# Optimization experiments

Measured on AMD Instinct MI355X. Metric: run time of the kernel, lower is better.

## Reference

```python
import jax, jax.numpy as jnp
import numpy as np

EMBED = 384
HEADS = 6
HEAD_SIZE = EMBED // HEADS
EPS = 1e-5


def _layernorm(x, g, b):
    mu = jnp.mean(x, axis=-1, keepdims=True)
    var = jnp.mean(jnp.square(x - mu), axis=-1, keepdims=True)
    return (x - mu) * jax.lax.rsqrt(var + EPS) * g + b


def setup_inputs() -> dict:
    key = jax.random.key(0)
    ks = jax.random.split(key, 16)
    B, T = 64, 256
    s_in = 1.0 / np.sqrt(EMBED)
    return {
        "x": jax.random.normal(ks[0], (B, T, EMBED), dtype=jnp.float32),
        # per-head q/k/v projections, stacked over heads: [H, C, D]
        "Wq": jax.random.normal(ks[1], (HEADS, EMBED, HEAD_SIZE), dtype=jnp.float32) * s_in,
        "bq": jnp.zeros((HEADS, HEAD_SIZE), dtype=jnp.float32),
        "Wk": jax.random.normal(ks[2], (HEADS, EMBED, HEAD_SIZE), dtype=jnp.float32) * s_in,
        "bk": jnp.zeros((HEADS, HEAD_SIZE), dtype=jnp.float32),
        "Wv": jax.random.normal(ks[3], (HEADS, EMBED, HEAD_SIZE), dtype=jnp.float32) * s_in,
        "bv": jnp.zeros((HEADS, HEAD_SIZE), dtype=jnp.float32),
        "Wp": jax.random.normal(ks[4], (EMBED, EMBED), dtype=jnp.float32) * s_in,
        "bp": jnp.zeros((EMBED,), dtype=jnp.float32),
        "W1": jax.random.normal(ks[5], (EMBED, EMBED), dtype=jnp.float32) * s_in,
        "b1": jnp.zeros((EMBED,), dtype=jnp.float32),
        "W2": jax.random.normal(ks[6], (EMBED, EMBED), dtype=jnp.float32) * s_in,
        "b2": jnp.zeros((EMBED,), dtype=jnp.float32),
        "ln1_g": jnp.ones((EMBED,), dtype=jnp.float32),
        "ln1_b": jnp.zeros((EMBED,), dtype=jnp.float32),
        "ln2_g": jnp.ones((EMBED,), dtype=jnp.float32),
        "ln2_b": jnp.zeros((EMBED,), dtype=jnp.float32),
    }


def reference(x, Wq, bq, Wk, bk, Wv, bv, Wp, bp, W1, b1, W2, b2,
              ln1_g, ln1_b, ln2_g, ln2_b):
    B, T, C = x.shape
    h = _layernorm(x, ln1_g, ln1_b)
    # batched per-head projections: [B,H,T,D]
    q = jnp.einsum('btc,hcd->bhtd', h, Wq) + bq[None, :, None, :]
    k = jnp.einsum('btc,hcd->bhtd', h, Wk) + bk[None, :, None, :]
    v = jnp.einsum('btc,hcd->bhtd', h, Wv) + bv[None, :, None, :]
    # NOTE: original scales by embed_size**0.5 (C=384), not head_size.
    wei = jnp.einsum('bhtd,bhsd->bhts', q, k) / jnp.sqrt(jnp.float32(C))
    causal = jnp.tril(jnp.ones((T, T), dtype=bool))
    wei = jnp.where(causal[None, None], wei, -jnp.inf)
    wei = jax.nn.softmax(wei, axis=-1)  # dropout = identity in eval
    attn = jnp.einsum('bhts,bhsd->bhtd', wei, v)  # [B,H,T,D]
    # concat heads in head order -> [B,T,C]
    attn = attn.transpose(0, 2, 1, 3).reshape(B, T, C)
    x = x + attn @ Wp + bp
    h2 = _layernorm(x, ln2_g, ln2_b)
    ff = jax.nn.relu(h2 @ W1 + b1) @ W2 + b2
    return x + ff
```

## Files before the change

### kernel.cpp

```cpp
#include <hip/hip_runtime.h>

typedef _Float16 f16;
typedef _Float16 half8 __attribute__((ext_vector_type(8)));
typedef _Float16 half4v __attribute__((ext_vector_type(4)));
typedef float floatx4 __attribute__((ext_vector_type(4)));

#define B_ 64
#define T_ 256
#define C_ 384
#define H_ 6
#define D_ 64
#define NROWS (B_*T_)

typedef __attribute__((address_space(3))) void lds_void_t;
typedef const __attribute__((address_space(1))) void gvoid_t;

__device__ __forceinline__ void g2lds16(const void* g, void* l) {
  __builtin_amdgcn_global_load_lds((gvoid_t*)g, (lds_void_t*)l, 16, 0, 0);
}

__global__ __launch_bounds__(256) void prep_ln_kernel(
    const float* __restrict__ Wq, const float* __restrict__ Wk, const float* __restrict__ Wv,
    const float* __restrict__ bq, const float* __restrict__ bk, const float* __restrict__ bv,
    const float* __restrict__ Wp, const float* __restrict__ W1, const float* __restrict__ W2,
    f16* __restrict__ Wqkv_t, f16* __restrict__ Wp_t, f16* __restrict__ W1_t, f16* __restrict__ W2_t,
    float* __restrict__ bqkv,
    const float* __restrict__ x, const float* __restrict__ gamma, const float* __restrict__ beta,
    f16* __restrict__ hout)
{
  const int bid = blockIdx.x;
  const int tid = threadIdx.x;
  if (bid >= 217) {
    int row = (bid - 217) * 4 + (tid >> 6);
    int lane = tid & 63;
    const float* xr = x + (size_t)row * 384;
    float v[6]; float s = 0.f;
#pragma unroll
    for (int j = 0; j < 6; j++) { v[j] = xr[lane + 64*j]; s += v[j]; }
#pragma unroll
    for (int m = 1; m < 64; m <<= 1) s += __shfl_xor(s, m);
    float mu = s * (1.f/384.f);
    float var = 0.f;
#pragma unroll
    for (int j = 0; j < 6; j++) { float d = v[j]-mu; var += d*d; }
#pragma unroll
    for (int m = 1; m < 64; m <<= 1) var += __shfl_xor(var, m);
    float rs = rsqrtf(var * (1.f/384.f) + 1e-5f);
    f16* orow = hout + (size_t)row*384;
#pragma unroll
    for (int j = 0; j < 6; j++) {
      int col = lane + 64*j;
      orow[col] = (f16)((v[j]-mu)*rs*gamma[col] + beta[col]);
    }
    return;
  }
  if (bid == 216) {
    for (int i = tid; i < 1152; i += 256) {
      float v;
      if (i < 384)      v = bq[i];
      else if (i < 768) v = bk[i - 384];
      else              v = bv[i - 768];
      bqkv[i] = v;
    }
    return;
  }
  __shared__ __align__(16) float tile[64*68];
  const float* src; int srcStride; f16* dst;
  if (bid < 108) {
    int mat = bid / 36, rem = bid - mat*36;
    int h = rem / 6, kt = rem - h*6;
    const float* W = (mat == 0) ? Wq : (mat == 1) ? Wk : Wv;
    src = W + (size_t)(h*384 + kt*64)*64;
    srcStride = 64;
    dst = Wqkv_t + (size_t)(mat*384 + h*64)*384 + kt*64;
  } else {
    int b2 = bid - 108;
    int mat = b2 / 36, rem = b2 - mat*36;
    int kt = rem / 6, ct = rem - kt*6;
    const float* W = (mat == 0) ? Wp : (mat == 1) ? W1 : W2;
    src = W + (size_t)(kt*64)*384 + ct*64;
    srcStride = 384;
    f16* O = (mat == 0) ? Wp_t : (mat == 1) ? W1_t : W2_t;
    dst = O + (size_t)(ct*64)*384 + kt*64;
  }
#pragma unroll
  for (int i = 0; i < 4; i++) {
    int idx = i*256 + tid;
    int r = idx >> 4, c4 = idx & 15;
    float4 v = *(const float4*)(src + (size_t)r*srcStride + c4*4);
    *(float4*)(&tile[r*68 + c4*4]) = v;
  }
  __syncthreads();
#pragma unroll
  for (int i = 0; i < 4; i++) {
    int idx = i*256 + tid;
    int d = idx >> 4, k4 = idx & 15;
    half4v o;
#pragma unroll
    for (int j = 0; j < 4; j++) o[j] = (f16)tile[(k4*4 + j)*68 + d];
    *(half4v*)(dst + (size_t)d*384 + k4*4) = o;
  }
}

__global__ __launch_bounds__(256) void gemm_qkv_kernel(
    const f16* __restrict__ A, const f16* __restrict__ Bt,
    const float* __restrict__ bias, f16* __restrict__ outp, int ldo)
{
  __shared__ __align__(16) f16 As[2][128*32];
  __shared__ __align__(16) f16 Bs[2][128*32];
  const int tid = threadIdx.x;
  const int lane = tid & 63, w = tid >> 6;
  const int wm = w >> 1, wn = w & 1;
  const int q = lane >> 4, c15 = lane & 15;
  const long row0 = (long)blockIdx.x * 128;
  const long col0 = (long)blockIdx.y * 128;
  floatx4 acc[4][4] = {};

  const int c0 = tid,        r0c = c0 >> 2, p0 = c0 & 3, g0 = p0 ^ ((r0c >> 1) & 3);
  const int c1 = 256 + tid,  r1c = c1 >> 2, p1 = c1 & 3, g1 = p1 ^ ((r1c >> 1) & 3);
  const f16* Arow0 = A  + (row0 + r0c)*384 + g0*8;
  const f16* Arow1 = A  + (row0 + r1c)*384 + g1*8;
  const f16* Brow0 = Bt + (col0 + r0c)*384 + g0*8;
  const f16* Brow1 = Bt + (col0 + r1c)*384 + g1*8;
  const int dof0 = (w*64)*8, dof1 = (256 + w*64)*8;

  for (int k0 = 0; k0 < 384; k0 += 64) {
#pragma unroll
    for (int hf = 0; hf < 2; hf++) {
      int kk = k0 + hf*32;
      g2lds16(Arow0 + kk, &As[hf][dof0]);
      g2lds16(Arow1 + kk, &As[hf][dof1]);
      g2lds16(Brow0 + kk, &Bs[hf][dof0]);
      g2lds16(Brow1 + kk, &Bs[hf][dof1]);
    }
    __syncthreads();
#pragma unroll
    for (int hf = 0; hf < 2; hf++) {
      half8 af[4], bf[4];
#pragma unroll
      for (int mi = 0; mi < 4; mi++) {
        int r = wm*64 + mi*16 + c15;
        int ph = q ^ ((r >> 1) & 3);
        af[mi] = *(const half8*)(&As[hf][r*32 + ph*8]);
      }
#pragma unroll
      for (int ni = 0; ni < 4; ni++) {
        int r = wn*64 + ni*16 + c15;
        int ph = q ^ ((r >> 1) & 3);
        bf[ni] = *(const half8*)(&Bs[hf][r*32 + ph*8]);
      }
#pragma unroll
      for (int mi = 0; mi < 4; mi++)
#pragma unroll
        for (int ni = 0; ni < 4; ni++)
          acc[mi][ni] = __builtin_amdgcn_mfma_f32_16x16x32_f16(af[mi], bf[ni], acc[mi][ni], 0, 0, 0);
    }
    __syncthreads();
  }

#pragma unroll
  for (int ni = 0; ni < 4; ni++) {
    long col = col0 + wn*64 + ni*16 + c15;
    float bv = bias[col];
#pragma unroll
    for (int mi = 0; mi < 4; mi++) {
      long rowb = row0 + wm*64 + mi*16 + q*4;
#pragma unroll
      for (int r = 0; r < 4; r++) {
        float vo = acc[mi][ni][r] + bv;
        outp[(rowb + r) * (long)ldo + col] = (f16)vo;
      }
    }
  }
}

__global__ __launch_bounds__(512, 2) void attn_kernel(const f16* __restrict__ qkv,
                                                      f16* __restrict__ attn_out)
{
  __shared__ __align__(16) char kvbuf[32768];
  __shared__ __align__(16) f16 Pbuf[8][16*64];
  f16* Ks = (f16*)kvbuf;
  unsigned int* vTw = (unsigned int*)kvbuf;
  f16* vT = (f16*)kvbuf;

  const int tid = threadIdx.x;
  const int bid = blockIdx.x;
  const int bh = bid >> 1, qt2 = bid & 1;
  const int b = bh / 6, h = bh - b*6;
  const f16* qp = qkv + (size_t)b*256*1152 + h*64;
  const f16* kp = qp + 384;
  const f16* vp = qp + 768;
  const int lane = tid & 63, w = tid >> 6;
  const int q = lane >> 4, c15 = lane & 15;

  {
    const int iters = (qt2 + 1) * 2;
    for (int i = 0; i < iters; i++) {
      int pc = i*512 + tid;
      int rc = pc >> 3, p = pc & 7;
      int c = p ^ (rc & 7);
      g2lds16(kp + (size_t)rc*1152 + c*8, (char*)kvbuf + (size_t)(i*512 + w*64)*16);
    }
  }

  const int nmax = qt2*8 + w;
  const int trow0 = qt2*128 + w*16;
  const f16* qrow = qp + (size_t)(trow0 + c15)*1152 + q*8;
  half8 aq0 = *(const half8*)(qrow);
  half8 aq1 = *(const half8*)(qrow + 32);

  __syncthreads();

  floatx4 sacc[16];
  __builtin_amdgcn_s_setprio(1);
#pragma unroll
  for (int ni = 0; ni < 16; ni++) {
    if (ni <= nmax) {
      int s = ni*16 + c15;
      const f16* kr = Ks + s*64;
      int p0 = q ^ (s & 7);
      half8 b0 = *(const half8*)(kr + p0*8);
      half8 b1 = *(const half8*)(kr + (p0 ^ 4)*8);
      floatx4 a = {0.f, 0.f, 0.f, 0.f};
      a = __builtin_amdgcn_mfma_f32_16x16x32_f16(aq0, b0, a, 0, 0, 0);
      a = __builtin_amdgcn_mfma_f32_16x16x32_f16(aq1, b1, a, 0, 0, 0);
      sacc[ni] = a;
    }
  }
  __builtin_amdgcn_s_setprio(0);
  __syncthreads();

  half8 va[2], vb[2];
#pragma unroll
  for (int i = 0; i < 2; i++) {
    if (i <= qt2) {
      int idx = i*512 + tid;
      int sp = idx >> 3, part = idx & 7;
      const f16* v0 = vp + (size_t)(2*sp)*1152 + part*8;
      va[i] = *(const half8*)(v0);
      vb[i] = *(const half8*)(v0 + 1152);
    }
  }

  const float scale = 0.051031036307982884f;
  float mx[4] = {-1e30f, -1e30f, -1e30f, -1e30f};
#pragma unroll
  for (int ni = 0; ni < 16; ni++) {
    if (ni < nmax) {
#pragma unroll
      for (int r = 0; r < 4; r++) { float v = sacc[ni][r]*scale; sacc[ni][r] = v; mx[r] = fmaxf(mx[r], v); }
    } else if (ni == nmax) {
#pragma unroll
      for (int r = 0; r < 4; r++) {
        float v = sacc[ni][r]*scale;
        v = (c15 <= q*4 + r) ? v : -1e30f;
        sacc[ni][r] = v; mx[r] = fmaxf(mx[r], v);
      }
    }
  }
#pragma unroll
  for (int r = 0; r < 4; r++) {
    mx[r] = fmaxf(mx[r], __shfl_xor(mx[r], 1));
    mx[r] = fmaxf(mx[r], __shfl_xor(mx[r], 2));
    mx[r] = fmaxf(mx[r], __shfl_xor(mx[r], 4));
    mx[r] = fmaxf(mx[r], __shfl_xor(mx[r], 8));
  }
  float l[4] = {0.f, 0.f, 0.f, 0.f};
#pragma unroll
  for (int ni = 0; ni < 16; ni++) {
    if (ni <= nmax) {
#pragma unroll
      for (int r = 0; r < 4; r++) { float p = __expf(sacc[ni][r] - mx[r]); sacc[ni][r] = p; l[r] += p; }
    }
  }
#pragma unroll
  for (int r = 0; r < 4; r++) {
    l[r] += __shfl_xor(l[r], 1);
    l[r] += __shfl_xor(l[r], 2);
    l[r] += __shfl_xor(l[r], 4);
    l[r] += __shfl_xor(l[r], 8);
  }

#pragma unroll
  for (int i = 0; i < 2; i++) {
    if (i <= qt2) {
      int idx = i*512 + tid;
      int sp = idx >> 3, part = idx & 7;
      int csp = sp >> 2, spw = sp & 3;
#pragma unroll
      for (int j = 0; j < 8; j++) {
        int d = part*8 + j;
        int swz = (d & 15) ^ (d >> 3);
        int p = csp ^ swz;
        union { struct { f16 lo, hi; } s; unsigned int u; } pk;
        pk.s.lo = va[i][j]; pk.s.hi = vb[i][j];
        vTw[d*128 + p*4 + spw] = pk.u;
      }
    }
  }
  __syncthreads();

  f16* Pw = &Pbuf[w][0];
  floatx4 oacc[4] = {};
  const int kend_w = (nmax + 1) * 16;
#pragma unroll
  for (int ch = 0; ch < 4; ch++) {
    if (ch*64 < kend_w) {
#pragma unroll
      for (int nl = 0; nl < 4; nl++) {
        int ni = ch*4 + nl;
        if (ni <= nmax) {
#pragma unroll
          for (int r = 0; r < 4; r++) {
            int row = q*4 + r;
            int colp = nl*16 + c15;
            int php = (colp >> 3) ^ (row & 7);
            Pw[row*64 + php*8 + (colp & 7)] = (f16)sacc[ni][r];
          }
        } else if (ni == nmax + 1) {
#pragma unroll
          for (int r = 0; r < 4; r++) {
            int row = q*4 + r;
            int colp = nl*16 + c15;
            int php = (colp >> 3) ^ (row & 7);
            Pw[row*64 + php*8 + (colp & 7)] = (f16)0.f;
          }
        }
      }
      __builtin_amdgcn_s_setprio(1);
#pragma unroll
      for (int kc = 0; kc < 2; kc++) {
        if (ch*64 + kc*32 < kend_w) {
          int pc = (kc*4 + q) ^ (c15 & 7);
          half8 ap = *(const half8*)(Pw + c15*64 + pc*8);
          int sc = ch*8 + kc*4 + q;
#pragma unroll
          for (int nt = 0; nt < 4; nt++) {
            int d = nt*16 + c15;
            int swz = (d & 15) ^ (d >> 3);
            half8 bv = *(const half8*)(vT + d*256 + ((sc ^ swz))*8);
            oacc[nt] = __builtin_amdgcn_mfma_f32_16x16x32_f16(ap, bv, oacc[nt], 0, 0, 0);
          }
        }
      }
      __builtin_amdgcn_s_setprio(0);
    }
  }

  float rl[4];
#pragma unroll
  for (int r = 0; r < 4; r++) rl[r] = 1.0f / l[r];
#pragma unroll
  for (int nt = 0; nt < 4; nt++) {
#pragma unroll
    for (int r = 0; r < 4; r++) {
      int t = trow0 + q*4 + r;
      int d = nt*16 + c15;
      attn_out[(size_t)(b*256 + t)*384 + h*64 + d] = (f16)(oacc[nt][r] * rl[r]);
    }
  }
}

__global__ __launch_bounds__(512, 2) void tail_kernel(
    const f16* __restrict__ A, const f16* __restrict__ WpT,
    const f16* __restrict__ W1T, const f16* __restrict__ W2T,
    const float* __restrict__ bp, const float* __restrict__ b1, const float* __restrict__ b2,
    const float* __restrict__ x, const float* __restrict__ g2, const float* __restrict__ be2,
    float* __restrict__ out)
{
  __shared__ __align__(16) f16 As[2][64*32];
  __shared__ __align__(16) f16 Bs[2][384*32];
  __shared__ __align__(16) f16 h2b[12][64*32];
  __shared__ __align__(16) f16 midb[12][64*32];
  __shared__ float lnred[2][64][4];
  __shared__ float lnmv[2][64];

  const int tid = threadIdx.x;
  const int lane = tid & 63, w = tid >> 6;
  const int wm = w >> 2, wn = w & 3;
  const int q = lane >> 4, c15 = lane & 15;
  const long row0 = (long)blockIdx.x * 64;

  const int cA = w*64 + lane;
  const int rA = cA >> 2, pA_ = cA & 3, gA = pA_ ^ ((rA >> 1) & 3);
  const f16* srcA = A + (row0 + rA)*384 + gA*8;
  auto boff = [&](int cb) -> long {
    int rc = cb >> 2, p = cb & 3, g = p ^ ((rc >> 1) & 3);
    return (long)rc*384 + g*8;
  };
  const long offBa0 = boff((w >= 4 ? (w-4) : 0)*64 + lane);
  const long offBa1 = boff(256 + w*64 + lane);
  const long offBa2 = boff(768 + w*64 + lane);
  const long offBa3 = boff(1280 + (w < 4 ? w : 0)*64 + lane);
  const long offBp0 = boff(w*64 + lane);
  const long offBp1 = boff(512 + w*64 + lane);
  const long offBp2 = boff(1024 + w*64 + lane);

  floatx4 acc[2][6] = {};

#define T_STAGE_A(buf, kk) do { \
    if (w < 4) { \
      g2lds16(srcA + (kk), &As[buf][(w*64)*8]); \
      g2lds16(WpT + offBa3 + (kk), &Bs[buf][(1280 + w*64)*8]); \
    } else { \
      g2lds16(WpT + offBa0 + (kk), &Bs[buf][((w-4)*64)*8]); \
    } \
    g2lds16(WpT + offBa1 + (kk), &Bs[buf][(256 + w*64)*8]); \
    g2lds16(WpT + offBa2 + (kk), &Bs[buf][(768 + w*64)*8]); \
  } while (0)

#define T_STAGE_B(buf, kk, BT) do { \
    g2lds16(BT + offBp0 + (kk), &Bs[buf][(w*64)*8]); \
    g2lds16(BT + offBp1 + (kk), &Bs[buf][(512 + w*64)*8]); \
    g2lds16(BT + offBp2 + (kk), &Bs[buf][(1024 + w*64)*8]); \
  } while (0)

#define T_COMP(ABUF_EXPR, buf) do { \
    half8 af[2], bf[6]; \
    _Pragma("unroll") \
    for (int mi = 0; mi < 2; mi++) { \
      int r = wm*32 + mi*16 + c15; \
      int ph = q ^ ((r >> 1) & 3); \
      af[mi] = *(const half8*)(&(ABUF_EXPR)[r*32 + ph*8]); \
    } \
    _Pragma("unroll") \
    for (int ni = 0; ni < 6; ni++) { \
      int rb = wn*96 + ni*16 + c15; \
      int phb = q ^ ((rb >> 1) & 3); \
      bf[ni] = *(const half8*)(&Bs[buf][rb*32 + phb*8]); \
    } \
    _Pragma("unroll") \
    for (int mi = 0; mi < 2; mi++) \
      _Pragma("unroll") \
      for (int ni = 0; ni < 6; ni++) \
        acc[mi][ni] = __builtin_amdgcn_mfma_f32_16x16x32_f16(af[mi], bf[ni], acc[mi][ni], 0, 0, 0); \
  } while (0)

  T_STAGE_A(0, 0);
  __syncthreads();
#pragma unroll
  for (int t = 0; t < 11; ++t) {
    T_STAGE_A((t + 1) & 1, (t + 1) * 32);
    T_COMP(As[t & 1], t & 1);
    __syncthreads();
  }
  T_COMP(As[1], 1);

  float vals[2][6][4];
  {
    float colb[6], cg[6], cb2[6];
#pragma unroll
    for (int ni = 0; ni < 6; ni++) {
      int col = wn*96 + ni*16 + c15;
      colb[ni] = bp[col]; cg[ni] = g2[col]; cb2[ni] = be2[col];
    }
#pragma unroll
    for (int mi = 0; mi < 2; mi++) {
#pragma unroll
      for (int rr = 0; rr < 4; rr++) {
        long row = row0 + wm*32 + mi*16 + q*4 + rr;
#pragma unroll
        for (int ni = 0; ni < 6; ni++) {
          int col = wn*96 + ni*16 + c15;
          float v = acc[mi][ni][rr] + colb[ni] + x[row*384 + col];
          vals[mi][ni][rr] = v;
        }
      }
    }
#pragma unroll
    for (int mi = 0; mi < 2; mi++) {
#pragma unroll
      for (int rr = 0; rr < 4; rr++) {
        float s = 0.f, s2 = 0.f;
#pragma unroll
        for (int ni = 0; ni < 6; ni++) { float v = vals[mi][ni][rr]; s += v; s2 += v*v; }
        s  += __shfl_xor(s, 1);  s  += __shfl_xor(s, 2);  s  += __shfl_xor(s, 4);  s  += __shfl_xor(s, 8);
        s2 += __shfl_xor(s2, 1); s2 += __shfl_xor(s2, 2); s2 += __shfl_xor(s2, 4); s2 += __shfl_xor(s2, 8);
        if (c15 == 0) {
          int lr = wm*32 + mi*16 + q*4 + rr;
          lnred[0][lr][wn] = s;
          lnred[1][lr][wn] = s2;
        }
      }
    }
    __syncthreads();
    if (tid < 64) {
      float s = 0.f, s2 = 0.f;
#pragma unroll
      for (int j = 0; j < 4; j++) { s += lnred[0][tid][j]; s2 += lnred[1][tid][j]; }
      float mu = s * (1.f/384.f);
      float var = s2 * (1.f/384.f) - mu*mu;
      lnmv[0][tid] = mu;
      lnmv[1][tid] = rsqrtf(var + 1e-5f);
    }
    __syncthreads();
#pragma unroll
    for (int mi = 0; mi < 2; mi++) {
#pragma unroll
      for (int rr = 0; rr < 4; rr++) {
        int lr = wm*32 + mi*16 + q*4 + rr;
        float mu = lnmv[0][lr], rs = lnmv[1][lr];
        int s_ = (lr >> 1) & 3;
#pragma unroll
        for (int ni = 0; ni < 6; ni++) {
          int cc = wn*96 + ni*16 + c15;
          float hv = (vals[mi][ni][rr] - mu)*rs*cg[ni] + cb2[ni];
          int chunk = cc >> 5, kk2 = cc & 31;
          int pos = ((kk2 >> 3) ^ s_)*8 + (kk2 & 7);
          h2b[chunk][lr*32 + pos] = (f16)hv;
        }
      }
    }
  }
  T_STAGE_B(0, 0, W1T);
  __syncthreads();

#pragma unroll
  for (int mi = 0; mi < 2; mi++)
#pragma unroll
    for (int ni = 0; ni < 6; ni++)
      acc[mi][ni] = floatx4{0.f, 0.f, 0.f, 0.f};
#pragma unroll
  for (int t = 0; t < 11; ++t) {
    T_STAGE_B((t + 1) & 1, (t + 1) * 32, W1T);
    T_COMP(h2b[t], t & 1);
    __syncthreads();
  }
  T_COMP(h2b[11], 1);

  {
    float colb[6];
#pragma unroll
    for (int ni = 0; ni < 6; ni++) colb[ni] = b1[wn*96 + ni*16 + c15];
#pragma unroll
    for (int mi = 0; mi < 2; mi++) {
#pragma unroll
      for (int rr = 0; rr < 4; rr++) {
        int lr = wm*32 + mi*16 + q*4 + rr;
        int s_ = (lr >> 1) & 3;
#pragma unroll
        for (int ni = 0; ni < 6; ni++) {
          int cc = wn*96 + ni*16 + c15;
          float v = acc[mi][ni][rr] + colb[ni];
          v = v > 0.f ? v : 0.f;
          int chunk = cc >> 5, kk2 = cc & 31;
          int pos = ((kk2 >> 3) ^ s_)*8 + (kk2 & 7);
          midb[chunk][lr*32 + pos] = (f16)v;
        }
      }
    }
  }
  T_STAGE_B(0, 0, W2T);
  __syncthreads();

#pragma unroll
  for (int mi = 0; mi < 2; mi++)
#pragma unroll
    for (int ni = 0; ni < 6; ni++)
      acc[mi][ni] = floatx4{0.f, 0.f, 0.f, 0.f};
#pragma unroll
  for (int t = 0; t < 11; ++t) {
    T_STAGE_B((t + 1) & 1, (t + 1) * 32, W2T);
    T_COMP(midb[t], t & 1);
    __syncthreads();
  }
  T_COMP(midb[11], 1);

  {
    float colb[6];
#pragma unroll
    for (int ni = 0; ni < 6; ni++) colb[ni] = b2[wn*96 + ni*16 + c15];
#pragma unroll
    for (int mi = 0; mi < 2; mi++) {
#pragma unroll
      for (int rr = 0; rr < 4; rr++) {
        long row = row0 + wm*32 + mi*16 + q*4 + rr;
#pragma unroll
        for (int ni = 0; ni < 6; ni++) {
          int col = wn*96 + ni*16 + c15;
          out[row*384 + col] = acc[mi][ni][rr] + colb[ni] + vals[mi][ni][rr];
        }
      }
    }
  }

#undef T_STAGE_A
#undef T_STAGE_B
#undef T_COMP
}

extern "C" void kernel_launch(void* const* d_in, const int* in_sizes, int n_in,
                              void* d_out, int out_size, void* d_ws, size_t ws_size,
                              hipStream_t stream) {
  const float* x   = (const float*)d_in[0];
  const float* Wq  = (const float*)d_in[1];
  const float* bq  = (const float*)d_in[2];
  const float* Wk  = (const float*)d_in[3];
  const float* bk  = (const float*)d_in[4];
  const float* Wv  = (const float*)d_in[5];
  const float* bv  = (const float*)d_in[6];
  const float* Wp  = (const float*)d_in[7];
  const float* bp  = (const float*)d_in[8];
  const float* W1  = (const float*)d_in[9];
  const float* b1  = (const float*)d_in[10];
  const float* W2  = (const float*)d_in[11];
  const float* b2  = (const float*)d_in[12];
  const float* g1  = (const float*)d_in[13];
  const float* be1 = (const float*)d_in[14];
  const float* g2  = (const float*)d_in[15];
  const float* be2 = (const float*)d_in[16];

  char* ws = (char*)d_ws;
  size_t off = 0;
  auto alloc = [&](size_t bytes) -> void* {
    void* p = ws + off;
    off += (bytes + 255) & ~(size_t)255;
    return p;
  };
  f16*   Wqkv_t = (f16*)  alloc(1152*384*sizeof(f16));
  f16*   Wp_t   = (f16*)  alloc(384*384*sizeof(f16));
  f16*   W1_t   = (f16*)  alloc(384*384*sizeof(f16));
  f16*   W2_t   = (f16*)  alloc(384*384*sizeof(f16));
  float* bqkv   = (float*)alloc(1152*sizeof(float));
  f16*   h      = (f16*)  alloc((size_t)NROWS*384*sizeof(f16));
  f16*   qkv    = (f16*)  alloc((size_t)NROWS*1152*sizeof(f16));
  f16*   attnb  = (f16*)  alloc((size_t)NROWS*384*sizeof(f16));

  prep_ln_kernel<<<217 + NROWS/4, 256, 0, stream>>>(Wq, Wk, Wv, bq, bk, bv, Wp, W1, W2,
                                                    Wqkv_t, Wp_t, W1_t, W2_t, bqkv,
                                                    x, g1, be1, h);
  gemm_qkv_kernel<<<dim3(128, 9), 256, 0, stream>>>(h, Wqkv_t, bqkv, qkv, 1152);
  attn_kernel<<<B_*H_*2, 512, 0, stream>>>(qkv, attnb);
  tail_kernel<<<NROWS/64, 512, 0, stream>>>(attnb, Wp_t, W1_t, W2_t, bp, b1, b2,
                                            x, g2, be2, (float*)d_out);
}
```

Measured before the change: 189.7 us.

## Restructure tail kernel with K=64 stages, shared row buffer, early prefetch

Measured after the change: 184.1 us. -3.0%, faster.

```diff
diff --git a/kernel.cpp b/kernel.cpp
--- a/kernel.cpp
+++ b/kernel.cpp
@@ -368,10 +368,8 @@
     const float* __restrict__ x, const float* __restrict__ g2, const float* __restrict__ be2,
     float* __restrict__ out)
 {
-  __shared__ __align__(16) f16 As[2][64*32];
-  __shared__ __align__(16) f16 Bs[2][384*32];
-  __shared__ __align__(16) f16 h2b[12][64*32];
-  __shared__ __align__(16) f16 midb[12][64*32];
+  __shared__ __align__(16) f16 rowbuf[12*64*32];
+  __shared__ __align__(16) f16 Bs[2][384*64];
   __shared__ float lnred[2][64][4];
   __shared__ float lnmv[2][64];
 
@@ -381,70 +379,84 @@
   const int q = lane >> 4, c15 = lane & 15;
   const long row0 = (long)blockIdx.x * 64;
 
-  const int cA = w*64 + lane;
-  const int rA = cA >> 2, pA_ = cA & 3, gA = pA_ ^ ((rA >> 1) & 3);
-  const f16* srcA = A + (row0 + rA)*384 + gA*8;
-  auto boff = [&](int cb) -> long {
-    int rc = cb >> 2, p = cb & 3, g = p ^ ((rc >> 1) & 3);
-    return (long)rc*384 + g*8;
-  };
-  const long offBa0 = boff((w >= 4 ? (w-4) : 0)*64 + lane);
-  const long offBa1 = boff(256 + w*64 + lane);
-  const long offBa2 = boff(768 + w*64 + lane);
-  const long offBa3 = boff(1280 + (w < 4 ? w : 0)*64 + lane);
-  const long offBp0 = boff(w*64 + lane);
-  const long offBp1 = boff(512 + w*64 + lane);
-  const long offBp2 = boff(1024 + w*64 + lane);
+  long offA[6];
+#pragma unroll
+  for (int i = 0; i < 6; i++) {
+    int cb = i*512 + tid;
+    int kc = cb >> 8, c2 = cb & 255;
+    int rA = c2 >> 2, pA = c2 & 3, gA = pA ^ ((rA >> 1) & 3);
+    offA[i] = (row0 + rA)*384 + kc*32 + gA*8;
+  }
+  long offB[6];
+#pragma unroll
+  for (int i = 0; i < 6; i++) {
+    int cb = i*512 + tid;
+    int rc = cb >> 3, r3 = cb & 7;
+    int hh = r3 >> 2, p = r3 & 3, g = p ^ ((rc >> 1) & 3);
+    offB[i] = (long)rc*384 + hh*32 + g*8;
+  }
 
   floatx4 acc[2][6] = {};
 
-#define T_STAGE_A(buf, kk) do { \
-    if (w < 4) { \
-      g2lds16(srcA + (kk), &As[buf][(w*64)*8]); \
-      g2lds16(WpT + offBa3 + (kk), &Bs[buf][(1280 + w*64)*8]); \
-    } else { \
-      g2lds16(WpT + offBa0 + (kk), &Bs[buf][((w-4)*64)*8]); \
-    } \
-    g2lds16(WpT + offBa1 + (kk), &Bs[buf][(256 + w*64)*8]); \
-    g2lds16(WpT + offBa2 + (kk), &Bs[buf][(768 + w*64)*8]); \
+#define T_STAGE_AFULL() do { \
+    _Pragma("unroll") \
+    for (int i = 0; i < 6; i++) \
+      g2lds16(A + offA[i], (char*)rowbuf + (size_t)(i*512 + w*64)*16); \
   } while (0)
 
 #define T_STAGE_B(buf, kk, BT) do { \
-    g2lds16(BT + offBp0 + (kk), &Bs[buf][(w*64)*8]); \
-    g2lds16(BT + offBp1 + (kk), &Bs[buf][(512 + w*64)*8]); \
-    g2lds16(BT + offBp2 + (kk), &Bs[buf][(1024 + w*64)*8]); \
+    _Pragma("unroll") \
+    for (int i = 0; i < 6; i++) \
+      g2lds16(BT + offB[i] + (kk), (char*)(&Bs[buf][0]) + (size_t)(i*512 + w*64)*16); \
   } while (0)
 
-#define T_COMP(ABUF_EXPR, buf) do { \
-    half8 af[2], bf[6]; \
+#define T_COMP64(a0, buf) do { \
+    half8 af[2][2], bf[2][6]; \
     _Pragma("unroll") \
-    for (int mi = 0; mi < 2; mi++) { \
-      int r = wm*32 + mi*16 + c15; \
-      int ph = q ^ ((r >> 1) & 3); \
-      af[mi] = *(const half8*)(&(ABUF_EXPR)[r*32 + ph*8]); \
+    for (int ks = 0; ks < 2; ks++) { \
+      _Pragma("unroll") \
+      for (int mi = 0; mi < 2; mi++) { \
+        int r = wm*32 + mi*16 + c15; \
+        int ph = q ^ ((r >> 1) & 3); \
+        af[ks][mi] = *(const half8*)(&rowbuf[((a0) + ks)*2048 + r*32 + ph*8]); \
+      } \
+      _Pragma("unroll") \
+      for (int ni = 0; ni < 6; ni++) { \
+        int rb = wn*96 + ni*16 + c15; \
+        int phb = q ^ ((rb >> 1) & 3); \
+        bf[ks][ni] = *(const half8*)(&Bs[buf][rb*64 + ks*32 + phb*8]); \
+      } \
     } \
     _Pragma("unroll") \
-    for (int ni = 0; ni < 6; ni++) { \
-      int rb = wn*96 + ni*16 + c15; \
-      int phb = q ^ ((rb >> 1) & 3); \
-      bf[ni] = *(const half8*)(&Bs[buf][rb*32 + phb*8]); \
-    } \
-    _Pragma("unroll") \
-    for (int mi = 0; mi < 2; mi++) \
+    for (int ks = 0; ks < 2; ks++) \
       _Pragma("unroll") \
-      for (int ni = 0; ni < 6; ni++) \
-        acc[mi][ni] = __builtin_amdgcn_mfma_f32_16x16x32_f16(af[mi], bf[ni], acc[mi][ni], 0, 0, 0); \
+      for (int mi = 0; mi < 2; mi++) \
+        _Pragma("unroll") \
+        for (int ni = 0; ni < 6; ni++) \
+          acc[mi][ni] = __builtin_amdgcn_mfma_f32_16x16x32_f16(af[ks][mi], bf[ks][ni], acc[mi][ni], 0, 0, 0); \
   } while (0)
 
-  T_STAGE_A(0, 0);
-  __syncthreads();
-#pragma unroll
-  for (int t = 0; t < 11; ++t) {
-    T_STAGE_A((t + 1) & 1, (t + 1) * 32);
-    T_COMP(As[t & 1], t & 1);
+  T_STAGE_AFULL();
+  T_STAGE_B(0, 0, WpT);
+  float xv[2][6][4];
+#pragma unroll
+  for (int mi = 0; mi < 2; mi++)
+#pragma unroll
+    for (int rr = 0; rr < 4; rr++) {
+      long row = row0 + wm*32 + mi*16 + q*4 + rr;
+#pragma unroll
+      for (int ni = 0; ni < 6; ni++)
+        xv[mi][ni][rr] = x[row*384 + wn*96 + ni*16 + c15];
+    }
+  __syncthreads();
+#pragma unroll
+  for (int t = 0; t < 5; ++t) {
+    T_STAGE_B((t + 1) & 1, (t + 1) * 64, WpT);
+    T_COMP64(2*t, t & 1);
     __syncthreads();
   }
-  T_COMP(As[1], 1);
+  T_COMP64(10, 1);
+  T_STAGE_B(0, 0, W1T);
 
   float vals[2][6][4];
   {
@@ -455,18 +467,12 @@
       colb[ni] = bp[col]; cg[ni] = g2[col]; cb2[ni] = be2[col];
     }
 #pragma unroll
-    for (int mi = 0; mi < 2; mi++) {
-#pragma unroll
-      for (int rr = 0; rr < 4; rr++) {
-        long row = row0 + wm*32 + mi*16 + q*4 + rr;
-#pragma unroll
-        for (int ni = 0; ni < 6; ni++) {
-          int col = wn*96 + ni*16 + c15;
-          float v = acc[mi][ni][rr] + colb[ni] + x[row*384 + col];
-          vals[mi][ni][rr] = v;
-        }
-      }
-    }
+    for (int mi = 0; mi < 2; mi++)
+#pragma unroll
+      for (int rr = 0; rr < 4; rr++)
+#pragma unroll
+        for (int ni = 0; ni < 6; ni++)
+          vals[mi][ni][rr] = acc[mi][ni][rr] + colb[ni] + xv[mi][ni][rr];
 #pragma unroll
     for (int mi = 0; mi < 2; mi++) {
 #pragma unroll
@@ -507,12 +513,11 @@
           float hv = (vals[mi][ni][rr] - mu)*rs*cg[ni] + cb2[ni];
           int chunk = cc >> 5, kk2 = cc & 31;
           int pos = ((kk2 >> 3) ^ s_)*8 + (kk2 & 7);
-          h2b[chunk][lr*32 + pos] = (f16)hv;
+          rowbuf[chunk*2048 + lr*32 + pos] = (f16)hv;
         }
       }
     }
   }
-  T_STAGE_B(0, 0, W1T);
   __syncthreads();
 
 #pragma unroll
@@ -521,12 +526,14 @@
     for (int ni = 0; ni < 6; ni++)
       acc[mi][ni] = floatx4{0.f, 0.f, 0.f, 0.f};
 #pragma unroll
-  for (int t = 0; t < 11; ++t) {
-    T_STAGE_B((t + 1) & 1, (t + 1) * 32, W1T);
-    T_COMP(h2b[t], t & 1);
+  for (int t = 0; t < 5; ++t) {
+    T_STAGE_B((t + 1) & 1, (t + 1) * 64, W1T);
+    T_COMP64(2*t, t & 1);
     __syncthreads();
   }
-  T_COMP(h2b[11], 1);
+  T_COMP64(10, 1);
+  T_STAGE_B(0, 0, W2T);
+  __syncthreads();
 
   {
     float colb[6];
@@ -545,12 +552,11 @@
           v = v > 0.f ? v : 0.f;
           int chunk = cc >> 5, kk2 = cc & 31;
           int pos = ((kk2 >> 3) ^ s_)*8 + (kk2 & 7);
-          midb[chunk][lr*32 + pos] = (f16)v;
+          rowbuf[chunk*2048 + lr*32 + pos] = (f16)v;
         }
       }
     }
   }
-  T_STAGE_B(0, 0, W2T);
   __syncthreads();
 
 #pragma unroll
@@ -559,12 +565,12 @@
     for (int ni = 0; ni < 6; ni++)
       acc[mi][ni] = floatx4{0.f, 0.f, 0.f, 0.f};
 #pragma unroll
-  for (int t = 0; t < 11; ++t) {
-    T_STAGE_B((t + 1) & 1, (t + 1) * 32, W2T);
-    T_COMP(midb[t], t & 1);
+  for (int t = 0; t < 5; ++t) {
+    T_STAGE_B((t + 1) & 1, (t + 1) * 64, W2T);
+    T_COMP64(2*t, t & 1);
     __syncthreads();
   }
-  T_COMP(midb[11], 1);
+  T_COMP64(10, 1);
 
   {
     float colb[6];
@@ -584,9 +590,9 @@
     }
   }
 
-#undef T_STAGE_A
+#undef T_STAGE_AFULL
 #undef T_STAGE_B
-#undef T_COMP
+#undef T_COMP64
 }
 
 extern "C" void kernel_launch(void* const* d_in, const int* in_sizes, int n_in,
```
